# Kernel optimization log

Measured on AMD Instinct MI355X. Metric: run time of the kernel, lower is better.

The kernel has to match this reference:

```python
import jax, jax.numpy as jnp
import numpy as np

B, IN, H, OUT, N = 2048, 512, 512, 256, 32768

def setup_inputs() -> dict:
    key = jax.random.key(0)
    ks = jax.random.split(key, 12)
    s = 1.0 / np.sqrt(H)
    inp = {
        'x': jax.random.normal(ks[0], (B, IN), jnp.float32),
        'Wih0': jax.random.uniform(ks[1], (3 * H, IN), jnp.float32, -s, s),
        'Whh0': jax.random.uniform(ks[2], (3 * H, H), jnp.float32, -s, s),
        'bih0': jax.random.uniform(ks[3], (3 * H,), jnp.float32, -s, s),
        'bhh0': jax.random.uniform(ks[4], (3 * H,), jnp.float32, -s, s),
        'Wih1': jax.random.uniform(ks[5], (3 * H, H), jnp.float32, -s, s),
        'Whh1': jax.random.uniform(ks[6], (3 * H, H), jnp.float32, -s, s),
        'bih1': jax.random.uniform(ks[7], (3 * H,), jnp.float32, -s, s),
        'bhh1': jax.random.uniform(ks[8], (3 * H,), jnp.float32, -s, s),
        'Wout': jax.random.uniform(ks[9], (OUT, H), jnp.float32, -s, s),
        'bout': jax.random.uniform(ks[10], (OUT,), jnp.float32, -s, s),
        'pre_set_idx': jnp.sort(jax.random.randint(ks[11], (N,), 0, B)),
    }
    return inp


def _gru_layer(seq, Wih, Whh, bih, bhh):
    # seq: [B, T, D]; PyTorch GRU gate order: r, z, n
    h_dim = Whh.shape[1]
    xp = jnp.einsum('btd,gd->btg', seq, Wih) + bih  # [B, T, 3H]
    xr, xz, xn = jnp.split(xp, 3, axis=-1)
    Whr, Whz, Whn = jnp.split(Whh, 3, axis=0)
    bhr, bhz, bhn = jnp.split(bhh, 3)

    def step(h, xs):
        xr_t, xz_t, xn_t = xs
        r = jax.nn.sigmoid(xr_t + h @ Whr.T + bhr)
        z = jax.nn.sigmoid(xz_t + h @ Whz.T + bhz)
        n = jnp.tanh(xn_t + r * (h @ Whn.T + bhn))
        h_new = (1.0 - z) * n + z * h
        return h_new, h_new

    h0 = jnp.zeros((seq.shape[0], h_dim), seq.dtype)
    xs = (xr.transpose(1, 0, 2), xz.transpose(1, 0, 2), xn.transpose(1, 0, 2))
    _, ys = jax.lax.scan(step, h0, xs)  # ys: [T, B, H]
    return ys.transpose(1, 0, 2)


def reference(x, Wih0, Whh0, bih0, bhh0, Wih1, Whh1, bih1, bhh1, Wout, bout, pre_set_idx):
    psi_np = np.asarray(pre_set_idx)
    counts_np = np.bincount(psi_np, minlength=B)
    T = int(counts_np.max())  # scipy mode(...).count == max count (static w.r.t. seed)

    # replicate the single-step input T times (original cat loop)
    x_seq = jnp.broadcast_to(x[:, None, :], (B, T, x.shape[1]))
    y0 = _gru_layer(x_seq, Wih0, Whh0, bih0, bhh0)
    y1 = _gru_layer(y0, Wih1, Whh1, bih1, bhh1)  # [B, T, H]

    # masked gather: for batch i, keep first cnt[i] timesteps (pre_set_idx is sorted)
    counts = jnp.asarray(counts_np)
    starts = jnp.concatenate([jnp.zeros(1, counts.dtype), jnp.cumsum(counts)[:-1]])
    rank = jnp.arange(N) - starts[pre_set_idx]  # position within each group
    gather_idx = pre_set_idx * T + rank
    flat = y1.reshape(-1, H)  # [B*T, H]
    sel = flat[gather_idx]  # [N, H]
    return sel @ Wout.T + bout  # [N, OUT]
```

## Files before the change

### kernel.cpp

```cpp
#include <hip/hip_runtime.h>
#include <math.h>

#define Bn   2048
#define Hd   512
#define H3   1536
#define OUTD 256
#define Nn   32768
#define TMAX 48
#define Kd   512

typedef __attribute__((ext_vector_type(8))) short short8v;
typedef __attribute__((ext_vector_type(4))) float float4v;

__device__ __forceinline__ float sigm(float x) { return 1.0f / (1.0f + __expf(-x)); }

__device__ __forceinline__ short f2bf(float v) {
    union { float f; unsigned u; } a; a.f = v;
    unsigned r = a.u + 0x7fffu + ((a.u >> 16) & 1u);
    return (short)(r >> 16);
}
__device__ __forceinline__ float bf2f(short s) {
    union { float f; unsigned u; } a; a.u = ((unsigned)(unsigned short)s) << 16;
    return a.f;
}

__global__ void prologue(const int* __restrict__ psi, int* __restrict__ perm,
                         int* __restrict__ startsP, int* __restrict__ active) {
    __shared__ int hist[64];
    __shared__ int base[64];
    __shared__ int cur[64];
    __shared__ int cnt_s[Bn];
    __shared__ int start_s[Bn];
    const int tid = threadIdx.x;
    if (tid < 64) { hist[tid] = 0; cur[tid] = 0; }
    __syncthreads();
    for (int b = tid; b < Bn; b += 1024) {
        int lo = 0, hi = Nn;
        while (lo < hi) { int mid = (lo + hi) >> 1; if (psi[mid] < b) lo = mid + 1; else hi = mid; }
        int lb = lo;
        lo = 0; hi = Nn;
        while (lo < hi) { int mid = (lo + hi) >> 1; if (psi[mid] <= b) lo = mid + 1; else hi = mid; }
        int c = lo - lb;
        cnt_s[b] = c;
        start_s[b] = lb;
        atomicAdd(&hist[min(c, 63)], 1);
    }
    __syncthreads();
    if (tid == 0) {
        base[63] = 0;
        for (int c = 62; c >= 0; --c) base[c] = base[c + 1] + hist[c + 1];
    }
    __syncthreads();
    if (tid < 64) active[tid] = base[tid];
    for (int b = tid; b < Bn; b += 1024) {
        int c = min(cnt_s[b], 63);
        int pos = base[c] + atomicAdd(&cur[c], 1);
        perm[pos] = b;
        startsP[pos] = start_s[b];
    }
}

__global__ __launch_bounds__(256)
void split_kern(const float* __restrict__ src, short* __restrict__ hi,
                short* __restrict__ lo, int n) {
    int i = (blockIdx.x * 256 + threadIdx.x) * 4;
    if (i >= n) return;
    float4 v = *(const float4*)&src[i];
    float vv[4] = {v.x, v.y, v.z, v.w};
    short h4[4], l4[4];
    #pragma unroll
    for (int c = 0; c < 4; ++c) {
        short h = f2bf(vv[c]);
        h4[c] = h;
        l4[c] = f2bf(vv[c] - bf2f(h));
    }
    *(short4*)&hi[i] = make_short4(h4[0], h4[1], h4[2], h4[3]);
    *(short4*)&lo[i] = make_short4(l4[0], l4[1], l4[2], l4[3]);
}

__global__ __launch_bounds__(256)
void zeroh(short* __restrict__ a, short* __restrict__ b,
           short* __restrict__ c, short* __restrict__ d) {
    int i = (blockIdx.x * 256 + threadIdx.x) * 4;
    short4 z = make_short4(0, 0, 0, 0);
    *(short4*)&a[i] = z; *(short4*)&b[i] = z;
    *(short4*)&c[i] = z; *(short4*)&d[i] = z;
}

template<bool SPLIT_A>
__device__ __forceinline__ void gemm_tile(
    const short* __restrict__ Ahi, const short* __restrict__ Alo,
    const short* __restrict__ Whi, const short* __restrict__ Wlo,
    const float* __restrict__ bias, float* __restrict__ C,
    int m0, int n0, int ldC, short* lds) {
    short* ldsAhi = lds;
    short* ldsAlo = lds + 4096;
    short* ldsBhi = lds + 8192;
    short* ldsBlo = lds + 12288;
    const int tid = threadIdx.x;
    const int wid = tid >> 6, lane = tid & 63;
    const int wm = wid >> 1, wn = wid & 1;
    const int oi0 = tid * 2, oi1 = tid * 2 + 1;
    const int r0 = oi0 >> 2, c0 = oi0 & 3;
    const int r1 = oi1 >> 2, c1 = oi1 & 3;
    const int w0 = ((r0 >> 4) * 64 + (r0 & 15) + (c0 << 4)) * 8;
    const int w1 = ((r1 >> 4) * 64 + (r1 & 15) + (c1 << 4)) * 8;

    float4v acc[4][4] = {};
    int4 ah0, ah1, al0, al1, bh0, bh1, bl0, bl1;

#define LOADK(kt) do { const int k0 = (kt) * 32; \
    ah0 = *(const int4*)&Ahi[(size_t)(m0 + r0) * Kd + k0 + c0 * 8]; \
    ah1 = *(const int4*)&Ahi[(size_t)(m0 + r1) * Kd + k0 + c1 * 8]; \
    if constexpr (SPLIT_A) { \
        al0 = *(const int4*)&Alo[(size_t)(m0 + r0) * Kd + k0 + c0 * 8]; \
        al1 = *(const int4*)&Alo[(size_t)(m0 + r1) * Kd + k0 + c1 * 8]; } \
    bh0 = *(const int4*)&Whi[(size_t)(n0 + r0) * Kd + k0 + c0 * 8]; \
    bh1 = *(const int4*)&Whi[(size_t)(n0 + r1) * Kd + k0 + c1 * 8]; \
    bl0 = *(const int4*)&Wlo[(size_t)(n0 + r0) * Kd + k0 + c0 * 8]; \
    bl1 = *(const int4*)&Wlo[(size_t)(n0 + r1) * Kd + k0 + c1 * 8]; } while (0)

    LOADK(0);
    for (int kt = 0; kt < 16; ++kt) {
        __syncthreads();
        *(int4*)&ldsAhi[w0] = ah0; *(int4*)&ldsAhi[w1] = ah1;
        if constexpr (SPLIT_A) { *(int4*)&ldsAlo[w0] = al0; *(int4*)&ldsAlo[w1] = al1; }
        *(int4*)&ldsBhi[w0] = bh0; *(int4*)&ldsBhi[w1] = bh1;
        *(int4*)&ldsBlo[w0] = bl0; *(int4*)&ldsBlo[w1] = bl1;
        __syncthreads();
        if (kt < 15) LOADK(kt + 1);
        short8v afh[4], afl[4], bfh[4], bfl[4];
        #pragma unroll
        for (int mi = 0; mi < 4; ++mi) {
            afh[mi] = *(const short8v*)&ldsAhi[((wm * 4 + mi) * 64 + lane) * 8];
            if constexpr (SPLIT_A)
                afl[mi] = *(const short8v*)&ldsAlo[((wm * 4 + mi) * 64 + lane) * 8];
        }
        #pragma unroll
        for (int ni = 0; ni < 4; ++ni) {
            bfh[ni] = *(const short8v*)&ldsBhi[((wn * 4 + ni) * 64 + lane) * 8];
            bfl[ni] = *(const short8v*)&ldsBlo[((wn * 4 + ni) * 64 + lane) * 8];
        }
        #pragma unroll
        for (int mi = 0; mi < 4; ++mi)
            #pragma unroll
            for (int ni = 0; ni < 4; ++ni) {
                acc[mi][ni] = __builtin_amdgcn_mfma_f32_16x16x32_bf16(afh[mi], bfh[ni], acc[mi][ni], 0, 0, 0);
                acc[mi][ni] = __builtin_amdgcn_mfma_f32_16x16x32_bf16(afh[mi], bfl[ni], acc[mi][ni], 0, 0, 0);
                if constexpr (SPLIT_A)
                    acc[mi][ni] = __builtin_amdgcn_mfma_f32_16x16x32_bf16(afl[mi], bfh[ni], acc[mi][ni], 0, 0, 0);
            }
    }
#undef LOADK
    #pragma unroll
    for (int mi = 0; mi < 4; ++mi) {
        #pragma unroll
        for (int ni = 0; ni < 4; ++ni) {
            int row = m0 + wm * 64 + mi * 16 + ((lane >> 4) << 2);
            int col = n0 + wn * 64 + ni * 16 + (lane & 15);
            float bv = bias ? bias[col] : 0.0f;
            #pragma unroll
            for (int r = 0; r < 4; ++r)
                C[(size_t)(row + r) * ldC + col] = acc[mi][ni][r] + bv;
        }
    }
}

template<bool SPLIT_A>
__global__ __launch_bounds__(256)
void gemm_one(const short* __restrict__ Ahi, const short* __restrict__ Alo,
              const short* __restrict__ Whi, const short* __restrict__ Wlo,
              const float* __restrict__ bias, float* __restrict__ C, int ntn) {
    __shared__ short lds[16384];
    int m0 = (blockIdx.x / ntn) * 128, n0 = (blockIdx.x % ntn) * 128;
    gemm_tile<SPLIT_A>(Ahi, Alo, Whi, Wlo, bias, C, m0, n0, ntn * 128, lds);
}

__global__ __launch_bounds__(256)
void step_gemm(const short* __restrict__ h0hi, const short* __restrict__ h0lo,
               const short* __restrict__ h1hi, const short* __restrict__ h1lo,
               const short* __restrict__ Whh0hi, const short* __restrict__ Whh0lo,
               const short* __restrict__ Wih1hi, const short* __restrict__ Wih1lo,
               const short* __restrict__ Whh1hi, const short* __restrict__ Whh1lo,
               float* __restrict__ gg0, float* __restrict__ ggX1, float* __restrict__ ggH1,
               const int* __restrict__ active, int i) {
    __shared__ short lds[16384];
    const int part = blockIdx.x / 192;
    const int bid = blockIdx.x % 192;
    const int m0 = (bid / 12) * 128, n0 = (bid % 12) * 128;
    if (part == 0) {
        const int act = active[i];
        if (m0 >= act) return;
        gemm_tile<true>(h0hi, h0lo, Whh0hi, Whh0lo, nullptr, gg0, m0, n0, H3, lds);
    } else if (part == 1) {
        if (i < 1) return;
        const int act = active[i - 1];
        if (m0 >= act) return;
        gemm_tile<true>(h0hi, h0lo, Wih1hi, Wih1lo, nullptr, ggX1, m0, n0, H3, lds);
    } else {
        if (i < 1) return;
        const int act = active[i - 1];
        if (m0 >= act) return;
        gemm_tile<true>(h1hi, h1lo, Whh1hi, Whh1lo, nullptr, ggH1, m0, n0, H3, lds);
    }
}

__global__ __launch_bounds__(256)
void cell_step(const float* __restrict__ gg0, const float* __restrict__ ggX1,
               const float* __restrict__ ggH1, const float* __restrict__ xp0,
               const float* __restrict__ bhh0, const float* __restrict__ bih1,
               const float* __restrict__ bhh1,
               short* __restrict__ h0hi, short* __restrict__ h0lo,
               short* __restrict__ h1hi, short* __restrict__ h1lo,
               short* __restrict__ sel_h,
               const int* __restrict__ perm, const int* __restrict__ startsP,
               const int* __restrict__ active, int i) {
    const int part = blockIdx.x >> 10;
    const int idx = (((blockIdx.x & 1023) * 256) + threadIdx.x) * 4;
    const int m = idx >> 9;
    const int j = idx & 511;
    if (part == 0) {
        const int act = active[i];
        if (m >= act) return;
        const int bsrc = perm[m];
        float4 gr = *(const float4*)&gg0[(size_t)m * H3 + j];
        float4 gz = *(const float4*)&gg0[(size_t)m * H3 + 512 + j];
        float4 gn = *(const float4*)&gg0[(size_t)m * H3 + 1024 + j];
        float4 xr = *(const float4*)&xp0[(size_t)bsrc * H3 + j];
        float4 xz = *(const float4*)&xp0[(size_t)bsrc * H3 + 512 + j];
        float4 xn = *(const float4*)&xp0[(size_t)bsrc * H3 + 1024 + j];
        short4 hh = *(const short4*)&h0hi[(size_t)m * Hd + j];
        short4 hl = *(const short4*)&h0lo[(size_t)m * Hd + j];
        float grv[4] = {gr.x, gr.y, gr.z, gr.w}, gzv[4] = {gz.x, gz.y, gz.z, gz.w}, gnv[4] = {gn.x, gn.y, gn.z, gn.w};
        float xrv[4] = {xr.x, xr.y, xr.z, xr.w}, xzv[4] = {xz.x, xz.y, xz.z, xz.w}, xnv[4] = {xn.x, xn.y, xn.z, xn.w};
        short hhv[4] = {hh.x, hh.y, hh.z, hh.w}, hlv[4] = {hl.x, hl.y, hl.z, hl.w};
        short nh[4], nl[4];
        #pragma unroll
        for (int c = 0; c < 4; ++c) {
            float hp = bf2f(hhv[c]) + bf2f(hlv[c]);
            float r = sigm(xrv[c] + grv[c] + bhh0[j + c]);
            float z = sigm(xzv[c] + gzv[c] + bhh0[512 + j + c]);
            float n = tanhf(xnv[c] + r * (gnv[c] + bhh0[1024 + j + c]));
            float h = (1.0f - z) * n + z * hp;
            nh[c] = f2bf(h);
            nl[c] = f2bf(h - bf2f(nh[c]));
        }
        *(short4*)&h0hi[(size_t)m * Hd + j] = make_short4(nh[0], nh[1], nh[2], nh[3]);
        *(short4*)&h0lo[(size_t)m * Hd + j] = make_short4(nl[0], nl[1], nl[2], nl[3]);
    } else {
        if (i < 1) return;
        const int act = active[i - 1];
        if (m >= act) return;
        const int t = i - 1;
        float4 ar = *(const float4*)&ggX1[(size_t)m * H3 + j];
        float4 az = *(const float4*)&ggX1[(size_t)m * H3 + 512 + j];
        float4 an = *(const float4*)&ggX1[(size_t)m * H3 + 1024 + j];
        float4 br = *(const float4*)&ggH1[(size_t)m * H3 + j];
        float4 bz = *(const float4*)&ggH1[(size_t)m * H3 + 512 + j];
        float4 bn = *(const float4*)&ggH1[(size_t)m * H3 + 1024 + j];
        short4 hh = *(const short4*)&h1hi[(size_t)m * Hd + j];
        short4 hl = *(const short4*)&h1lo[(size_t)m * Hd + j];
        float arv[4] = {ar.x, ar.y, ar.z, ar.w}, azv[4] = {az.x, az.y, az.z, az.w}, anv[4] = {an.x, an.y, an.z, an.w};
        float brv[4] = {br.x, br.y, br.z, br.w}, bzv[4] = {bz.x, bz.y, bz.z, bz.w}, bnv[4] = {bn.x, bn.y, bn.z, bn.w};
        short hhv[4] = {hh.x, hh.y, hh.z, hh.w}, hlv[4] = {hl.x, hl.y, hl.z, hl.w};
        short nh[4], nl[4], sb[4];
        #pragma unroll
        for (int c = 0; c < 4; ++c) {
            float hp = bf2f(hhv[c]) + bf2f(hlv[c]);
            float r = sigm(arv[c] + bih1[j + c] + brv[c] + bhh1[j + c]);
            float z = sigm(azv[c] + bih1[512 + j + c] + bzv[c] + bhh1[512 + j + c]);
            float n = tanhf(anv[c] + bih1[1024 + j + c] + r * (bnv[c] + bhh1[1024 + j + c]));
            float h = (1.0f - z) * n + z * hp;
            nh[c] = f2bf(h);
            nl[c] = f2bf(h - bf2f(nh[c]));
            sb[c] = f2bf(h);
        }
        *(short4*)&h1hi[(size_t)m * Hd + j] = make_short4(nh[0], nh[1], nh[2], nh[3]);
        *(short4*)&h1lo[(size_t)m * Hd + j] = make_short4(nl[0], nl[1], nl[2], nl[3]);
        size_t orow = (size_t)startsP[m] + t;
        *(short4*)&sel_h[orow * Hd + j] = make_short4(sb[0], sb[1], sb[2], sb[3]);
    }
}

extern "C" void kernel_launch(void* const* d_in, const int* in_sizes, int n_in,
                              void* d_out, int out_size, void* d_ws, size_t ws_size,
                              hipStream_t stream) {
    (void)in_sizes; (void)n_in; (void)out_size; (void)ws_size;
    const float* x    = (const float*)d_in[0];
    const float* Wih0 = (const float*)d_in[1];
    const float* Whh0 = (const float*)d_in[2];
    const float* bih0 = (const float*)d_in[3];
    const float* bhh0 = (const float*)d_in[4];
    const float* Wih1 = (const float*)d_in[5];
    const float* Whh1 = (const float*)d_in[6];
    const float* bih1 = (const float*)d_in[7];
    const float* bhh1 = (const float*)d_in[8];
    const float* Wout = (const float*)d_in[9];
    const float* bout = (const float*)d_in[10];
    const int*   psi  = (const int*)d_in[11];
    float* out = (float*)d_out;

    char* p = (char*)d_ws;
    auto alloc = [&](size_t bytes) { char* r = p; p += (bytes + 255) & ~255ULL; return r; };
    short* xhi    = (short*)alloc((size_t)Bn * Kd * 2);
    short* xlo    = (short*)alloc((size_t)Bn * Kd * 2);
    short* Wih0hi = (short*)alloc((size_t)H3 * Kd * 2);
    short* Wih0lo = (short*)alloc((size_t)H3 * Kd * 2);
    short* Whh0hi = (short*)alloc((size_t)H3 * Kd * 2);
    short* Whh0lo = (short*)alloc((size_t)H3 * Kd * 2);
    short* Wih1hi = (short*)alloc((size_t)H3 * Kd * 2);
    short* Wih1lo = (short*)alloc((size_t)H3 * Kd * 2);
    short* Whh1hi = (short*)alloc((size_t)H3 * Kd * 2);
    short* Whh1lo = (short*)alloc((size_t)H3 * Kd * 2);
    short* Wouthi = (short*)alloc((size_t)OUTD * Kd * 2);
    short* Woutlo = (short*)alloc((size_t)OUTD * Kd * 2);
    float* xp0    = (float*)alloc((size_t)Bn * H3 * 4);
    float* gg0    = (float*)alloc((size_t)Bn * H3 * 4);
    float* ggX1   = (float*)alloc((size_t)Bn * H3 * 4);
    float* ggH1   = (float*)alloc((size_t)Bn * H3 * 4);
    short* h0hi   = (short*)alloc((size_t)Bn * Hd * 2);
    short* h0lo   = (short*)alloc((size_t)Bn * Hd * 2);
    short* h1hi   = (short*)alloc((size_t)Bn * Hd * 2);
    short* h1lo   = (short*)alloc((size_t)Bn * Hd * 2);
    short* sel_h  = (short*)alloc((size_t)Nn * Hd * 2);
    int* perm     = (int*)alloc(Bn * 4);
    int* startsP  = (int*)alloc(Bn * 4);
    int* active   = (int*)alloc(64 * 4);

    split_kern<<<1024, 256, 0, stream>>>(x, xhi, xlo, Bn * Kd);
    split_kern<<<768, 256, 0, stream>>>(Wih0, Wih0hi, Wih0lo, H3 * Kd);
    split_kern<<<768, 256, 0, stream>>>(Whh0, Whh0hi, Whh0lo, H3 * Kd);
    split_kern<<<768, 256, 0, stream>>>(Wih1, Wih1hi, Wih1lo, H3 * Kd);
    split_kern<<<768, 256, 0, stream>>>(Whh1, Whh1hi, Whh1lo, H3 * Kd);
    split_kern<<<128, 256, 0, stream>>>(Wout, Wouthi, Woutlo, OUTD * Kd);
    prologue<<<1, 1024, 0, stream>>>(psi, perm, startsP, active);
    zeroh<<<1024, 256, 0, stream>>>(h0hi, h0lo, h1hi, h1lo);

    gemm_one<true><<<192, 256, 0, stream>>>(xhi, xlo, Wih0hi, Wih0lo, bih0, xp0, 12);

    for (int i = 0; i <= TMAX; ++i) {
        step_gemm<<<576, 256, 0, stream>>>(h0hi, h0lo, h1hi, h1lo,
                                           Whh0hi, Whh0lo, Wih1hi, Wih1lo, Whh1hi, Whh1lo,
                                           gg0, ggX1, ggH1, active, i);
        cell_step<<<2048, 256, 0, stream>>>(gg0, ggX1, ggH1, xp0,
                                            bhh0, bih1, bhh1,
                                            h0hi, h0lo, h1hi, h1lo,
                                            sel_h, perm, startsP, active, i);
    }

    gemm_one<false><<<512, 256, 0, stream>>>(sel_h, nullptr, Wouthi, Woutlo, bout, out, 2);
}
```

Baseline: 1.553 ms.

## Fuse per-step GRU gate GEMMs with cell update using ping-pong hidden buffers

Replaces the separate step GEMM and elementwise cell kernels with one fused kernel per timestep. Each block computes the r, z and n gate tiles for a 32-column slice and applies the GRU update in registers, so the fp32 gate intermediates no longer round-trip through global memory. Layer-1 input and hidden weights for r/z are concatenated along K so one 1024-long reduction serves both. Hidden states are stored interleaved in double-buffered [B,1024] arrays, and x is pre-permuted so xp0 needs no per-step indirection. The cost is narrower N tiles per block, which means the A operand is reloaded more often and layer-1 blocks do twice as much K work as layer-0 blocks, giving uneven load.

```diff
diff --git a/kernel.cpp b/kernel.cpp
--- a/kernel.cpp
+++ b/kernel.cpp
@@ -23,6 +23,8 @@
     union { float f; unsigned u; } a; a.u = ((unsigned)(unsigned short)s) << 16;
     return a.f;
 }
+
+#define MF(acc, A, B) acc = __builtin_amdgcn_mfma_f32_16x16x32_bf16(A, B, acc, 0, 0, 0)
 
 __global__ void prologue(const int* __restrict__ psi, int* __restrict__ perm,
                          int* __restrict__ startsP, int* __restrict__ active) {
@@ -79,9 +81,49 @@
 }
 
 __global__ __launch_bounds__(256)
-void zeroh(short* __restrict__ a, short* __restrict__ b,
-           short* __restrict__ c, short* __restrict__ d) {
+void split_perm(const float* __restrict__ src, const int* __restrict__ perm,
+                short* __restrict__ hi, short* __restrict__ lo) {
     int i = (blockIdx.x * 256 + threadIdx.x) * 4;
+    int row = i >> 9, col = i & 511;
+    int srow = perm[row];
+    float4 v = *(const float4*)&src[(size_t)srow * 512 + col];
+    float vv[4] = {v.x, v.y, v.z, v.w};
+    short h4[4], l4[4];
+    #pragma unroll
+    for (int c = 0; c < 4; ++c) {
+        short h = f2bf(vv[c]);
+        h4[c] = h;
+        l4[c] = f2bf(vv[c] - bf2f(h));
+    }
+    *(short4*)&hi[i] = make_short4(h4[0], h4[1], h4[2], h4[3]);
+    *(short4*)&lo[i] = make_short4(l4[0], l4[1], l4[2], l4[3]);
+}
+
+__global__ __launch_bounds__(256)
+void pack_w1rz(const float* __restrict__ Wih1, const float* __restrict__ Whh1,
+               short* __restrict__ hi, short* __restrict__ lo) {
+    int i = (blockIdx.x * 256 + threadIdx.x) * 4;
+    int orow = i >> 10, k = i & 1023;
+    const float* s = (k < 512) ? &Wih1[(size_t)orow * 512 + k]
+                               : &Whh1[(size_t)orow * 512 + (k - 512)];
+    float4 v = *(const float4*)s;
+    float vv[4] = {v.x, v.y, v.z, v.w};
+    short h4[4], l4[4];
+    #pragma unroll
+    for (int c = 0; c < 4; ++c) {
+        short h = f2bf(vv[c]);
+        h4[c] = h;
+        l4[c] = f2bf(vv[c] - bf2f(h));
+    }
+    *(short4*)&hi[i] = make_short4(h4[0], h4[1], h4[2], h4[3]);
+    *(short4*)&lo[i] = make_short4(l4[0], l4[1], l4[2], l4[3]);
+}
+
+__global__ __launch_bounds__(256)
+void zero4(short* __restrict__ a, short* __restrict__ b,
+           short* __restrict__ c, short* __restrict__ d, int n) {
+    int i = (blockIdx.x * 256 + threadIdx.x) * 4;
+    if (i >= n) return;
     short4 z = make_short4(0, 0, 0, 0);
     *(short4*)&a[i] = z; *(short4*)&b[i] = z;
     *(short4*)&c[i] = z; *(short4*)&d[i] = z;
@@ -145,10 +187,9 @@
         for (int mi = 0; mi < 4; ++mi)
             #pragma unroll
             for (int ni = 0; ni < 4; ++ni) {
-                acc[mi][ni] = __builtin_amdgcn_mfma_f32_16x16x32_bf16(afh[mi], bfh[ni], acc[mi][ni], 0, 0, 0);
-                acc[mi][ni] = __builtin_amdgcn_mfma_f32_16x16x32_bf16(afh[mi], bfl[ni], acc[mi][ni], 0, 0, 0);
-                if constexpr (SPLIT_A)
-                    acc[mi][ni] = __builtin_amdgcn_mfma_f32_16x16x32_bf16(afl[mi], bfh[ni], acc[mi][ni], 0, 0, 0);
+                MF(acc[mi][ni], afh[mi], bfh[ni]);
+                MF(acc[mi][ni], afh[mi], bfl[ni]);
+                if constexpr (SPLIT_A) MF(acc[mi][ni], afl[mi], bfh[ni]);
             }
     }
 #undef LOADK
@@ -177,109 +218,194 @@
 }
 
 __global__ __launch_bounds__(256)
-void step_gemm(const short* __restrict__ h0hi, const short* __restrict__ h0lo,
-               const short* __restrict__ h1hi, const short* __restrict__ h1lo,
-               const short* __restrict__ Whh0hi, const short* __restrict__ Whh0lo,
-               const short* __restrict__ Wih1hi, const short* __restrict__ Wih1lo,
-               const short* __restrict__ Whh1hi, const short* __restrict__ Whh1lo,
-               float* __restrict__ gg0, float* __restrict__ ggX1, float* __restrict__ ggH1,
-               const int* __restrict__ active, int i) {
-    __shared__ short lds[16384];
-    const int part = blockIdx.x / 192;
-    const int bid = blockIdx.x % 192;
-    const int m0 = (bid / 12) * 128, n0 = (bid % 12) * 128;
+void fused_step(const short* __restrict__ OLDhi, const short* __restrict__ OLDlo,
+                short* __restrict__ NEWhi, short* __restrict__ NEWlo,
+                const short* __restrict__ W0hi, const short* __restrict__ W0lo,
+                const short* __restrict__ Wrzhi, const short* __restrict__ Wrzlo,
+                const short* __restrict__ Wnxhi, const short* __restrict__ Wnxlo,
+                const short* __restrict__ Wnhhi, const short* __restrict__ Wnhlo,
+                const float* __restrict__ xp0P, const float* __restrict__ bhh0,
+                const float* __restrict__ bih1, const float* __restrict__ bhh1,
+                short* __restrict__ sel_h, const int* __restrict__ startsP,
+                const int* __restrict__ active, int i) {
+    __shared__ short lds[14336];
+    const int tid = threadIdx.x;
+    const int bb = blockIdx.x;
+    const int part = (bb >= 256);
+    const int idx = bb & 255;
+    const int js = idx >> 4, mb = idx & 15;
+    const int m0 = mb * 128, j0 = js * 32;
+    const int wid = tid >> 6, lane = tid & 63;
+    const int wm = wid >> 1, wn = wid & 1;
+
+    short* ldsAhi = lds;
+    short* ldsAlo = lds + 4096;
+    short* ldsP   = lds + 8192;
+
+    const int oiA0 = tid * 2, oiA1 = tid * 2 + 1;
+    const int rA0 = oiA0 >> 2, cA0 = oiA0 & 3;
+    const int rA1 = oiA1 >> 2, cA1 = oiA1 & 3;
+    const int wA0 = ((rA0 >> 4) * 64 + (rA0 & 15) + (cA0 << 4)) * 8;
+    const int wA1 = ((rA1 >> 4) * 64 + (rA1 & 15) + (cA1 << 4)) * 8;
+
+    const short* aB0h = OLDhi + (size_t)(m0 + rA0) * 1024 + cA0 * 8;
+    const short* aB1h = OLDhi + (size_t)(m0 + rA1) * 1024 + cA1 * 8;
+    const short* aB0l = OLDlo + (size_t)(m0 + rA0) * 1024 + cA0 * 8;
+    const short* aB1l = OLDlo + (size_t)(m0 + rA1) * 1024 + cA1 * 8;
+
+    int wPq[3], pg[3], prw[3], poc[3];
+    #pragma unroll
+    for (int rep = 0; rep < 3; ++rep) {
+        int id2 = rep * 256 + tid;
+        int p = id2 >> 7, wi = id2 & 127;
+        int prow = wi >> 2, poct = wi & 3;
+        wPq[rep] = p * 1024 + ((prow >> 4) * 64 + (prow & 15) + (poct << 4)) * 8;
+        pg[rep] = p; prw[rep] = prow; poc[rep] = poct;
+    }
+
+    const int col = j0 + wn * 16 + (lane & 15);
+
+#define AFRAGS \
+    short8v afh[4], afl[4]; \
+    _Pragma("unroll") for (int mi = 0; mi < 4; ++mi) { \
+        afh[mi] = *(const short8v*)&ldsAhi[((wm * 4 + mi) * 64 + lane) * 8]; \
+        afl[mi] = *(const short8v*)&ldsAlo[((wm * 4 + mi) * 64 + lane) * 8]; }
+
+#define GATEB(ACC, G) { \
+    short8v bh = *(const short8v*)&ldsP[((G) * 2 + 0) * 1024 + (wn * 64 + lane) * 8]; \
+    short8v bl = *(const short8v*)&ldsP[((G) * 2 + 1) * 1024 + (wn * 64 + lane) * 8]; \
+    _Pragma("unroll") for (int mi = 0; mi < 4; ++mi) { \
+        MF(ACC[mi], afh[mi], bh); MF(ACC[mi], afh[mi], bl); MF(ACC[mi], afl[mi], bh); } }
+
     if (part == 0) {
         const int act = active[i];
         if (m0 >= act) return;
-        gemm_tile<true>(h0hi, h0lo, Whh0hi, Whh0lo, nullptr, gg0, m0, n0, H3, lds);
-    } else if (part == 1) {
-        if (i < 1) return;
-        const int act = active[i - 1];
-        if (m0 >= act) return;
-        gemm_tile<true>(h0hi, h0lo, Wih1hi, Wih1lo, nullptr, ggX1, m0, n0, H3, lds);
+        const short* pb[3];
+        #pragma unroll
+        for (int rep = 0; rep < 3; ++rep) {
+            const short* W = (pg[rep] & 1) ? W0lo : W0hi;
+            pb[rep] = W + (size_t)((pg[rep] >> 1) * 512 + j0 + prw[rep]) * 512 + poc[rep] * 8;
+        }
+        float4v aR[4] = {}, aZ[4] = {}, aN[4] = {};
+        int4 s0, s1, s2, s3, q0, q1, q2;
+        auto LOAD = [&](int kt) {
+            int k0 = kt * 32;
+            s0 = *(const int4*)(aB0h + k0); s1 = *(const int4*)(aB1h + k0);
+            s2 = *(const int4*)(aB0l + k0); s3 = *(const int4*)(aB1l + k0);
+            q0 = *(const int4*)(pb[0] + k0);
+            q1 = *(const int4*)(pb[1] + k0);
+            q2 = *(const int4*)(pb[2] + k0);
+        };
+        LOAD(0);
+        for (int kt = 0; kt < 16; ++kt) {
+            __syncthreads();
+            *(int4*)&ldsAhi[wA0] = s0; *(int4*)&ldsAhi[wA1] = s1;
+            *(int4*)&ldsAlo[wA0] = s2; *(int4*)&ldsAlo[wA1] = s3;
+            *(int4*)&ldsP[wPq[0]] = q0; *(int4*)&ldsP[wPq[1]] = q1; *(int4*)&ldsP[wPq[2]] = q2;
+            __syncthreads();
+            if (kt < 15) LOAD(kt + 1);
+            AFRAGS
+            GATEB(aR, 0)
+            GATEB(aZ, 1)
+            GATEB(aN, 2)
+        }
+        const float b_r = bhh0[col], b_z = bhh0[512 + col], b_n = bhh0[1024 + col];
+        #pragma unroll
+        for (int mi = 0; mi < 4; ++mi) {
+            int rowb = m0 + wm * 64 + mi * 16 + ((lane >> 4) << 2);
+            #pragma unroll
+            for (int r = 0; r < 4; ++r) {
+                int row = rowb + r;
+                float xr = xp0P[(size_t)row * H3 + col];
+                float xz = xp0P[(size_t)row * H3 + 512 + col];
+                float xn = xp0P[(size_t)row * H3 + 1024 + col];
+                float rr = sigm(xr + aR[mi][r] + b_r);
+                float zz = sigm(xz + aZ[mi][r] + b_z);
+                float nn = tanhf(xn + rr * (aN[mi][r] + b_n));
+                float hp = bf2f(OLDhi[(size_t)row * 1024 + col]) + bf2f(OLDlo[(size_t)row * 1024 + col]);
+                float h = (1.0f - zz) * nn + zz * hp;
+                short hh = f2bf(h);
+                NEWhi[(size_t)row * 1024 + col] = hh;
+                NEWlo[(size_t)row * 1024 + col] = f2bf(h - bf2f(hh));
+            }
+        }
     } else {
         if (i < 1) return;
         const int act = active[i - 1];
         if (m0 >= act) return;
-        gemm_tile<true>(h1hi, h1lo, Whh1hi, Whh1lo, nullptr, ggH1, m0, n0, H3, lds);
-    }
-}
-
-__global__ __launch_bounds__(256)
-void cell_step(const float* __restrict__ gg0, const float* __restrict__ ggX1,
-               const float* __restrict__ ggH1, const float* __restrict__ xp0,
-               const float* __restrict__ bhh0, const float* __restrict__ bih1,
-               const float* __restrict__ bhh1,
-               short* __restrict__ h0hi, short* __restrict__ h0lo,
-               short* __restrict__ h1hi, short* __restrict__ h1lo,
-               short* __restrict__ sel_h,
-               const int* __restrict__ perm, const int* __restrict__ startsP,
-               const int* __restrict__ active, int i) {
-    const int part = blockIdx.x >> 10;
-    const int idx = (((blockIdx.x & 1023) * 256) + threadIdx.x) * 4;
-    const int m = idx >> 9;
-    const int j = idx & 511;
-    if (part == 0) {
-        const int act = active[i];
-        if (m >= act) return;
-        const int bsrc = perm[m];
-        float4 gr = *(const float4*)&gg0[(size_t)m * H3 + j];
-        float4 gz = *(const float4*)&gg0[(size_t)m * H3 + 512 + j];
-        float4 gn = *(const float4*)&gg0[(size_t)m * H3 + 1024 + j];
-        float4 xr = *(const float4*)&xp0[(size_t)bsrc * H3 + j];
-        float4 xz = *(const float4*)&xp0[(size_t)bsrc * H3 + 512 + j];
-        float4 xn = *(const float4*)&xp0[(size_t)bsrc * H3 + 1024 + j];
-        short4 hh = *(const short4*)&h0hi[(size_t)m * Hd + j];
-        short4 hl = *(const short4*)&h0lo[(size_t)m * Hd + j];
-        float grv[4] = {gr.x, gr.y, gr.z, gr.w}, gzv[4] = {gz.x, gz.y, gz.z, gz.w}, gnv[4] = {gn.x, gn.y, gn.z, gn.w};
-        float xrv[4] = {xr.x, xr.y, xr.z, xr.w}, xzv[4] = {xz.x, xz.y, xz.z, xz.w}, xnv[4] = {xn.x, xn.y, xn.z, xn.w};
-        short hhv[4] = {hh.x, hh.y, hh.z, hh.w}, hlv[4] = {hl.x, hl.y, hl.z, hl.w};
-        short nh[4], nl[4];
-        #pragma unroll
-        for (int c = 0; c < 4; ++c) {
-            float hp = bf2f(hhv[c]) + bf2f(hlv[c]);
-            float r = sigm(xrv[c] + grv[c] + bhh0[j + c]);
-            float z = sigm(xzv[c] + gzv[c] + bhh0[512 + j + c]);
-            float n = tanhf(xnv[c] + r * (gnv[c] + bhh0[1024 + j + c]));
-            float h = (1.0f - z) * n + z * hp;
-            nh[c] = f2bf(h);
-            nl[c] = f2bf(h - bf2f(nh[c]));
-        }
-        *(short4*)&h0hi[(size_t)m * Hd + j] = make_short4(nh[0], nh[1], nh[2], nh[3]);
-        *(short4*)&h0lo[(size_t)m * Hd + j] = make_short4(nl[0], nl[1], nl[2], nl[3]);
-    } else {
-        if (i < 1) return;
-        const int act = active[i - 1];
-        if (m >= act) return;
         const int t = i - 1;
-        float4 ar = *(const float4*)&ggX1[(size_t)m * H3 + j];
-        float4 az = *(const float4*)&ggX1[(size_t)m * H3 + 512 + j];
-        float4 an = *(const float4*)&ggX1[(size_t)m * H3 + 1024 + j];
-        float4 br = *(const float4*)&ggH1[(size_t)m * H3 + j];
-        float4 bz = *(const float4*)&ggH1[(size_t)m * H3 + 512 + j];
-        float4 bn = *(const float4*)&ggH1[(size_t)m * H3 + 1024 + j];
-        short4 hh = *(const short4*)&h1hi[(size_t)m * Hd + j];
-        short4 hl = *(const short4*)&h1lo[(size_t)m * Hd + j];
-        float arv[4] = {ar.x, ar.y, ar.z, ar.w}, azv[4] = {az.x, az.y, az.z, az.w}, anv[4] = {an.x, an.y, an.z, an.w};
-        float brv[4] = {br.x, br.y, br.z, br.w}, bzv[4] = {bz.x, bz.y, bz.z, bz.w}, bnv[4] = {bn.x, bn.y, bn.z, bn.w};
-        short hhv[4] = {hh.x, hh.y, hh.z, hh.w}, hlv[4] = {hl.x, hl.y, hl.z, hl.w};
-        short nh[4], nl[4], sb[4];
-        #pragma unroll
-        for (int c = 0; c < 4; ++c) {
-            float hp = bf2f(hhv[c]) + bf2f(hlv[c]);
-            float r = sigm(arv[c] + bih1[j + c] + brv[c] + bhh1[j + c]);
-            float z = sigm(azv[c] + bih1[512 + j + c] + bzv[c] + bhh1[512 + j + c]);
-            float n = tanhf(anv[c] + bih1[1024 + j + c] + r * (bnv[c] + bhh1[1024 + j + c]));
-            float h = (1.0f - z) * n + z * hp;
-            nh[c] = f2bf(h);
-            nl[c] = f2bf(h - bf2f(nh[c]));
-            sb[c] = f2bf(h);
-        }
-        *(short4*)&h1hi[(size_t)m * Hd + j] = make_short4(nh[0], nh[1], nh[2], nh[3]);
-        *(short4*)&h1lo[(size_t)m * Hd + j] = make_short4(nl[0], nl[1], nl[2], nl[3]);
-        size_t orow = (size_t)startsP[m] + t;
-        *(short4*)&sel_h[orow * Hd + j] = make_short4(sb[0], sb[1], sb[2], sb[3]);
-    }
+        const short* pbRZ[3]; const short* pbNx[3]; const short* pbNh[3]; int isn[3];
+        #pragma unroll
+        for (int rep = 0; rep < 3; ++rep) {
+            int g = pg[rep] >> 1, hl = pg[rep] & 1;
+            isn[rep] = (g == 2);
+            const short* Wrz = hl ? Wrzlo : Wrzhi;
+            const short* Wx  = hl ? Wnxlo : Wnxhi;
+            const short* Wh  = hl ? Wnhlo : Wnhhi;
+            pbRZ[rep] = Wrz + (size_t)(min(g, 1) * 512 + j0 + prw[rep]) * 1024 + poc[rep] * 8;
+            pbNx[rep] = Wx + (size_t)(j0 + prw[rep]) * 512 + poc[rep] * 8;
+            pbNh[rep] = Wh + (size_t)(j0 + prw[rep]) * 512 + poc[rep] * 8;
+        }
+        float4v aR[4] = {}, aZ[4] = {}, aXn[4] = {}, aHn[4] = {};
+        int4 s0, s1, s2, s3, q0, q1, q2;
+        auto LOAD = [&](int kt) {
+            int k0 = kt * 32;
+            s0 = *(const int4*)(aB0h + k0); s1 = *(const int4*)(aB1h + k0);
+            s2 = *(const int4*)(aB0l + k0); s3 = *(const int4*)(aB1l + k0);
+            q0 = *(const int4*)(isn[0] ? ((kt < 16) ? pbNx[0] + k0 : pbNh[0] + (k0 - 512)) : pbRZ[0] + k0);
+            q1 = *(const int4*)(isn[1] ? ((kt < 16) ? pbNx[1] + k0 : pbNh[1] + (k0 - 512)) : pbRZ[1] + k0);
+            q2 = *(const int4*)(isn[2] ? ((kt < 16) ? pbNx[2] + k0 : pbNh[2] + (k0 - 512)) : pbRZ[2] + k0);
+        };
+        LOAD(0);
+        for (int kt = 0; kt < 16; ++kt) {
+            __syncthreads();
+            *(int4*)&ldsAhi[wA0] = s0; *(int4*)&ldsAhi[wA1] = s1;
+            *(int4*)&ldsAlo[wA0] = s2; *(int4*)&ldsAlo[wA1] = s3;
+            *(int4*)&ldsP[wPq[0]] = q0; *(int4*)&ldsP[wPq[1]] = q1; *(int4*)&ldsP[wPq[2]] = q2;
+            __syncthreads();
+            LOAD(kt + 1);
+            AFRAGS
+            GATEB(aR, 0)
+            GATEB(aZ, 1)
+            GATEB(aXn, 2)
+        }
+        for (int kt = 16; kt < 32; ++kt) {
+            __syncthreads();
+            *(int4*)&ldsAhi[wA0] = s0; *(int4*)&ldsAhi[wA1] = s1;
+            *(int4*)&ldsAlo[wA0] = s2; *(int4*)&ldsAlo[wA1] = s3;
+            *(int4*)&ldsP[wPq[0]] = q0; *(int4*)&ldsP[wPq[1]] = q1; *(int4*)&ldsP[wPq[2]] = q2;
+            __syncthreads();
+            if (kt < 31) LOAD(kt + 1);
+            AFRAGS
+            GATEB(aR, 0)
+            GATEB(aZ, 1)
+            GATEB(aHn, 2)
+        }
+        const float b_r = bih1[col] + bhh1[col];
+        const float b_z = bih1[512 + col] + bhh1[512 + col];
+        const float b_xn = bih1[1024 + col];
+        const float b_hn = bhh1[1024 + col];
+        #pragma unroll
+        for (int mi = 0; mi < 4; ++mi) {
+            int rowb = m0 + wm * 64 + mi * 16 + ((lane >> 4) << 2);
+            #pragma unroll
+            for (int r = 0; r < 4; ++r) {
+                int row = rowb + r;
+                float rr = sigm(aR[mi][r] + b_r);
+                float zz = sigm(aZ[mi][r] + b_z);
+                float nn = tanhf(aXn[mi][r] + b_xn + rr * (aHn[mi][r] + b_hn));
+                float hp = bf2f(OLDhi[(size_t)row * 1024 + 512 + col]) + bf2f(OLDlo[(size_t)row * 1024 + 512 + col]);
+                float h = (1.0f - zz) * nn + zz * hp;
+                short hh = f2bf(h);
+                NEWhi[(size_t)row * 1024 + 512 + col] = hh;
+                NEWlo[(size_t)row * 1024 + 512 + col] = f2bf(h - bf2f(hh));
+                if (row < act)
+                    sel_h[((size_t)startsP[row] + t) * Hd + col] = f2bf(h);
+            }
+        }
+    }
+#undef AFRAGS
+#undef GATEB
 }
 
 extern "C" void kernel_launch(void* const* d_in, const int* in_sizes, int n_in,
@@ -302,50 +428,52 @@
 
     char* p = (char*)d_ws;
     auto alloc = [&](size_t bytes) { char* r = p; p += (bytes + 255) & ~255ULL; return r; };
-    short* xhi    = (short*)alloc((size_t)Bn * Kd * 2);
-    short* xlo    = (short*)alloc((size_t)Bn * Kd * 2);
+    short* xPhi   = (short*)alloc((size_t)Bn * Kd * 2);
+    short* xPlo   = (short*)alloc((size_t)Bn * Kd * 2);
     short* Wih0hi = (short*)alloc((size_t)H3 * Kd * 2);
     short* Wih0lo = (short*)alloc((size_t)H3 * Kd * 2);
-    short* Whh0hi = (short*)alloc((size_t)H3 * Kd * 2);
-    short* Whh0lo = (short*)alloc((size_t)H3 * Kd * 2);
-    short* Wih1hi = (short*)alloc((size_t)H3 * Kd * 2);
-    short* Wih1lo = (short*)alloc((size_t)H3 * Kd * 2);
-    short* Whh1hi = (short*)alloc((size_t)H3 * Kd * 2);
-    short* Whh1lo = (short*)alloc((size_t)H3 * Kd * 2);
+    short* W0hi   = (short*)alloc((size_t)H3 * Kd * 2);
+    short* W0lo   = (short*)alloc((size_t)H3 * Kd * 2);
+    short* Wrzhi  = (short*)alloc((size_t)1024 * 1024 * 2);
+    short* Wrzlo  = (short*)alloc((size_t)1024 * 1024 * 2);
+    short* Wnxhi  = (short*)alloc((size_t)512 * 512 * 2);
+    short* Wnxlo  = (short*)alloc((size_t)512 * 512 * 2);
+    short* Wnhhi  = (short*)alloc((size_t)512 * 512 * 2);
+    short* Wnhlo  = (short*)alloc((size_t)512 * 512 * 2);
     short* Wouthi = (short*)alloc((size_t)OUTD * Kd * 2);
     short* Woutlo = (short*)alloc((size_t)OUTD * Kd * 2);
-    float* xp0    = (float*)alloc((size_t)Bn * H3 * 4);
-    float* gg0    = (float*)alloc((size_t)Bn * H3 * 4);
-    float* ggX1   = (float*)alloc((size_t)Bn * H3 * 4);
-    float* ggH1   = (float*)alloc((size_t)Bn * H3 * 4);
-    short* h0hi   = (short*)alloc((size_t)Bn * Hd * 2);
-    short* h0lo   = (short*)alloc((size_t)Bn * Hd * 2);
-    short* h1hi   = (short*)alloc((size_t)Bn * Hd * 2);
-    short* h1lo   = (short*)alloc((size_t)Bn * Hd * 2);
+    float* xp0P   = (float*)alloc((size_t)Bn * H3 * 4);
+    short* Aahi   = (short*)alloc((size_t)Bn * 1024 * 2);
+    short* Aalo   = (short*)alloc((size_t)Bn * 1024 * 2);
+    short* Abhi   = (short*)alloc((size_t)Bn * 1024 * 2);
+    short* Ablo   = (short*)alloc((size_t)Bn * 1024 * 2);
     short* sel_h  = (short*)alloc((size_t)Nn * Hd * 2);
     int* perm     = (int*)alloc(Bn * 4);
     int* startsP  = (int*)alloc(Bn * 4);
     int* active   = (int*)alloc(64 * 4);
 
-    split_kern<<<1024, 256, 0, stream>>>(x, xhi, xlo, Bn * Kd);
+    prologue<<<1, 1024, 0, stream>>>(psi, perm, startsP, active);
+    split_perm<<<1024, 256, 0, stream>>>(x, perm, xPhi, xPlo);
     split_kern<<<768, 256, 0, stream>>>(Wih0, Wih0hi, Wih0lo, H3 * Kd);
-    split_kern<<<768, 256, 0, stream>>>(Whh0, Whh0hi, Whh0lo, H3 * Kd);
-    split_kern<<<768, 256, 0, stream>>>(Wih1, Wih1hi, Wih1lo, H3 * Kd);
-    split_kern<<<768, 256, 0, stream>>>(Whh1, Whh1hi, Whh1lo, H3 * Kd);
+    split_kern<<<768, 256, 0, stream>>>(Whh0, W0hi, W0lo, H3 * Kd);
+    pack_w1rz<<<1024, 256, 0, stream>>>(Wih1, Whh1, Wrzhi, Wrzlo);
+    split_kern<<<256, 256, 0, stream>>>(Wih1 + (size_t)1024 * 512, Wnxhi, Wnxlo, 512 * 512);
+    split_kern<<<256, 256, 0, stream>>>(Whh1 + (size_t)1024 * 512, Wnhhi, Wnhlo, 512 * 512);
     split_kern<<<128, 256, 0, stream>>>(Wout, Wouthi, Woutlo, OUTD * Kd);
-    prologue<<<1, 1024, 0, stream>>>(psi, perm, startsP, active);
-    zeroh<<<1024, 256, 0, stream>>>(h0hi, h0lo, h1hi, h1lo);
-
-    gemm_one<true><<<192, 256, 0, stream>>>(xhi, xlo, Wih0hi, Wih0lo, bih0, xp0, 12);
+    zero4<<<2048, 256, 0, stream>>>(Aahi, Aalo, Abhi, Ablo, Bn * 1024);
+
+    gemm_one<true><<<192, 256, 0, stream>>>(xPhi, xPlo, Wih0hi, Wih0lo, bih0, xp0P, 12);
 
     for (int i = 0; i <= TMAX; ++i) {
-        step_gemm<<<576, 256, 0, stream>>>(h0hi, h0lo, h1hi, h1lo,
-                                           Whh0hi, Whh0lo, Wih1hi, Wih1lo, Whh1hi, Whh1lo,
-                                           gg0, ggX1, ggH1, active, i);
-        cell_step<<<2048, 256, 0, stream>>>(gg0, ggX1, ggH1, xp0,
-                                            bhh0, bih1, bhh1,
-                                            h0hi, h0lo, h1hi, h1lo,
-                                            sel_h, perm, startsP, active, i);
+        const short* OLDhi = (i & 1) ? Abhi : Aahi;
+        const short* OLDlo = (i & 1) ? Ablo : Aalo;
+        short* NEWhi = (i & 1) ? Aahi : Abhi;
+        short* NEWlo = (i & 1) ? Aalo : Ablo;
+        fused_step<<<512, 256, 0, stream>>>(OLDhi, OLDlo, NEWhi, NEWlo,
+                                            W0hi, W0lo, Wrzhi, Wrzlo,
+                                            Wnxhi, Wnxlo, Wnhhi, Wnhlo,
+                                            xp0P, bhh0, bih1, bhh1,
+                                            sel_h, startsP, active, i);
     }
 
     gemm_one<false><<<512, 256, 0, stream>>>(sel_h, nullptr, Wouthi, Woutlo, bout, out, 2);
```

New measurement: 1.766 ms. +13.7%, slower.

## Use 512-thread GEMM tiles and pre-permute x to drop gather in cell step

Applied to the files above, without the earlier changes.

The GEMM tile moves from 4 waves with 4x4 MFMA subtiles to 8 waves with 4x2 subtiles. Each thread now stages one 16-byte chunk per operand per k-step, and step_gemm and gemm_one launch with 512 threads. Separately, x is permuted by perm while it is split to bf16, so the layer-0 input projection comes out already in sorted row order and cell_step reads it directly instead of through perm. This trades per-wave register and accumulator pressure for more waves per block and removes an indirect load, but each wave now gets less B-fragment reuse.

```diff
diff --git a/kernel.cpp b/kernel.cpp
--- a/kernel.cpp
+++ b/kernel.cpp
@@ -23,6 +23,8 @@
     union { float f; unsigned u; } a; a.u = ((unsigned)(unsigned short)s) << 16;
     return a.f;
 }
+
+#define MF(acc, A, B) acc = __builtin_amdgcn_mfma_f32_16x16x32_bf16(A, B, acc, 0, 0, 0)
 
 __global__ void prologue(const int* __restrict__ psi, int* __restrict__ perm,
                          int* __restrict__ startsP, int* __restrict__ active) {
@@ -43,6 +45,7 @@
         int c = lo - lb;
         cnt_s[b] = c;
         start_s[b] = lb;
+        lmax:;
         atomicAdd(&hist[min(c, 63)], 1);
     }
     __syncthreads();
@@ -79,6 +82,25 @@
 }
 
 __global__ __launch_bounds__(256)
+void split_perm(const float* __restrict__ src, const int* __restrict__ perm,
+                short* __restrict__ hi, short* __restrict__ lo) {
+    int i = (blockIdx.x * 256 + threadIdx.x) * 4;
+    int row = i >> 9, col = i & 511;
+    int srow = perm[row];
+    float4 v = *(const float4*)&src[(size_t)srow * 512 + col];
+    float vv[4] = {v.x, v.y, v.z, v.w};
+    short h4[4], l4[4];
+    #pragma unroll
+    for (int c = 0; c < 4; ++c) {
+        short h = f2bf(vv[c]);
+        h4[c] = h;
+        l4[c] = f2bf(vv[c] - bf2f(h));
+    }
+    *(short4*)&hi[i] = make_short4(h4[0], h4[1], h4[2], h4[3]);
+    *(short4*)&lo[i] = make_short4(l4[0], l4[1], l4[2], l4[3]);
+}
+
+__global__ __launch_bounds__(256)
 void zeroh(short* __restrict__ a, short* __restrict__ b,
            short* __restrict__ c, short* __restrict__ d) {
     int i = (blockIdx.x * 256 + threadIdx.x) * 4;
@@ -99,37 +121,34 @@
     short* ldsBlo = lds + 12288;
     const int tid = threadIdx.x;
     const int wid = tid >> 6, lane = tid & 63;
-    const int wm = wid >> 1, wn = wid & 1;
-    const int oi0 = tid * 2, oi1 = tid * 2 + 1;
-    const int r0 = oi0 >> 2, c0 = oi0 & 3;
-    const int r1 = oi1 >> 2, c1 = oi1 & 3;
-    const int w0 = ((r0 >> 4) * 64 + (r0 & 15) + (c0 << 4)) * 8;
-    const int w1 = ((r1 >> 4) * 64 + (r1 & 15) + (c1 << 4)) * 8;
-
-    float4v acc[4][4] = {};
-    int4 ah0, ah1, al0, al1, bh0, bh1, bl0, bl1;
+    const int wm = wid >> 2, wn = wid & 3;
+    const int sr = tid >> 2, so = tid & 3;
+    const int wOff = ((sr >> 4) * 64 + (sr & 15) + (so << 4)) * 8;
+
+    const short* gAhi = Ahi + (size_t)(m0 + sr) * Kd + so * 8;
+    const short* gAlo = SPLIT_A ? (Alo + (size_t)(m0 + sr) * Kd + so * 8) : nullptr;
+    const short* gBhi = Whi + (size_t)(n0 + sr) * Kd + so * 8;
+    const short* gBlo = Wlo + (size_t)(n0 + sr) * Kd + so * 8;
+
+    float4v acc[4][2] = {};
+    int4 vah, val, vbh, vbl;
 
 #define LOADK(kt) do { const int k0 = (kt) * 32; \
-    ah0 = *(const int4*)&Ahi[(size_t)(m0 + r0) * Kd + k0 + c0 * 8]; \
-    ah1 = *(const int4*)&Ahi[(size_t)(m0 + r1) * Kd + k0 + c1 * 8]; \
-    if constexpr (SPLIT_A) { \
-        al0 = *(const int4*)&Alo[(size_t)(m0 + r0) * Kd + k0 + c0 * 8]; \
-        al1 = *(const int4*)&Alo[(size_t)(m0 + r1) * Kd + k0 + c1 * 8]; } \
-    bh0 = *(const int4*)&Whi[(size_t)(n0 + r0) * Kd + k0 + c0 * 8]; \
-    bh1 = *(const int4*)&Whi[(size_t)(n0 + r1) * Kd + k0 + c1 * 8]; \
-    bl0 = *(const int4*)&Wlo[(size_t)(n0 + r0) * Kd + k0 + c0 * 8]; \
-    bl1 = *(const int4*)&Wlo[(size_t)(n0 + r1) * Kd + k0 + c1 * 8]; } while (0)
+    vah = *(const int4*)(gAhi + k0); \
+    if constexpr (SPLIT_A) val = *(const int4*)(gAlo + k0); \
+    vbh = *(const int4*)(gBhi + k0); \
+    vbl = *(const int4*)(gBlo + k0); } while (0)
 
     LOADK(0);
     for (int kt = 0; kt < 16; ++kt) {
         __syncthreads();
-        *(int4*)&ldsAhi[w0] = ah0; *(int4*)&ldsAhi[w1] = ah1;
-        if constexpr (SPLIT_A) { *(int4*)&ldsAlo[w0] = al0; *(int4*)&ldsAlo[w1] = al1; }
-        *(int4*)&ldsBhi[w0] = bh0; *(int4*)&ldsBhi[w1] = bh1;
-        *(int4*)&ldsBlo[w0] = bl0; *(int4*)&ldsBlo[w1] = bl1;
+        *(int4*)&ldsAhi[wOff] = vah;
+        if constexpr (SPLIT_A) *(int4*)&ldsAlo[wOff] = val;
+        *(int4*)&ldsBhi[wOff] = vbh;
+        *(int4*)&ldsBlo[wOff] = vbl;
         __syncthreads();
         if (kt < 15) LOADK(kt + 1);
-        short8v afh[4], afl[4], bfh[4], bfl[4];
+        short8v afh[4], afl[4], bfh[2], bfl[2];
         #pragma unroll
         for (int mi = 0; mi < 4; ++mi) {
             afh[mi] = *(const short8v*)&ldsAhi[((wm * 4 + mi) * 64 + lane) * 8];
@@ -137,27 +156,26 @@
                 afl[mi] = *(const short8v*)&ldsAlo[((wm * 4 + mi) * 64 + lane) * 8];
         }
         #pragma unroll
-        for (int ni = 0; ni < 4; ++ni) {
-            bfh[ni] = *(const short8v*)&ldsBhi[((wn * 4 + ni) * 64 + lane) * 8];
-            bfl[ni] = *(const short8v*)&ldsBlo[((wn * 4 + ni) * 64 + lane) * 8];
+        for (int ni = 0; ni < 2; ++ni) {
+            bfh[ni] = *(const short8v*)&ldsBhi[((wn * 2 + ni) * 64 + lane) * 8];
+            bfl[ni] = *(const short8v*)&ldsBlo[((wn * 2 + ni) * 64 + lane) * 8];
         }
         #pragma unroll
         for (int mi = 0; mi < 4; ++mi)
             #pragma unroll
-            for (int ni = 0; ni < 4; ++ni) {
-                acc[mi][ni] = __builtin_amdgcn_mfma_f32_16x16x32_bf16(afh[mi], bfh[ni], acc[mi][ni], 0, 0, 0);
-                acc[mi][ni] = __builtin_amdgcn_mfma_f32_16x16x32_bf16(afh[mi], bfl[ni], acc[mi][ni], 0, 0, 0);
-                if constexpr (SPLIT_A)
-                    acc[mi][ni] = __builtin_amdgcn_mfma_f32_16x16x32_bf16(afl[mi], bfh[ni], acc[mi][ni], 0, 0, 0);
+            for (int ni = 0; ni < 2; ++ni) {
+                MF(acc[mi][ni], afh[mi], bfh[ni]);
+                MF(acc[mi][ni], afh[mi], bfl[ni]);
+                if constexpr (SPLIT_A) MF(acc[mi][ni], afl[mi], bfh[ni]);
             }
     }
 #undef LOADK
     #pragma unroll
     for (int mi = 0; mi < 4; ++mi) {
         #pragma unroll
-        for (int ni = 0; ni < 4; ++ni) {
+        for (int ni = 0; ni < 2; ++ni) {
             int row = m0 + wm * 64 + mi * 16 + ((lane >> 4) << 2);
-            int col = n0 + wn * 64 + ni * 16 + (lane & 15);
+            int col = n0 + wn * 32 + ni * 16 + (lane & 15);
             float bv = bias ? bias[col] : 0.0f;
             #pragma unroll
             for (int r = 0; r < 4; ++r)
@@ -167,7 +185,7 @@
 }
 
 template<bool SPLIT_A>
-__global__ __launch_bounds__(256)
+__global__ __launch_bounds__(512)
 void gemm_one(const short* __restrict__ Ahi, const short* __restrict__ Alo,
               const short* __restrict__ Whi, const short* __restrict__ Wlo,
               const float* __restrict__ bias, float* __restrict__ C, int ntn) {
@@ -176,7 +194,7 @@
     gemm_tile<SPLIT_A>(Ahi, Alo, Whi, Wlo, bias, C, m0, n0, ntn * 128, lds);
 }
 
-__global__ __launch_bounds__(256)
+__global__ __launch_bounds__(512)
 void step_gemm(const short* __restrict__ h0hi, const short* __restrict__ h0lo,
                const short* __restrict__ h1hi, const short* __restrict__ h1lo,
                const short* __restrict__ Whh0hi, const short* __restrict__ Whh0lo,
@@ -207,13 +225,13 @@
 
 __global__ __launch_bounds__(256)
 void cell_step(const float* __restrict__ gg0, const float* __restrict__ ggX1,
-               const float* __restrict__ ggH1, const float* __restrict__ xp0,
+               const float* __restrict__ ggH1, const float* __restrict__ xp0P,
                const float* __restrict__ bhh0, const float* __restrict__ bih1,
                const float* __restrict__ bhh1,
                short* __restrict__ h0hi, short* __restrict__ h0lo,
                short* __restrict__ h1hi, short* __restrict__ h1lo,
                short* __restrict__ sel_h,
-               const int* __restrict__ perm, const int* __restrict__ startsP,
+               const int* __restrict__ startsP,
                const int* __restrict__ active, int i) {
     const int part = blockIdx.x >> 10;
     const int idx = (((blockIdx.x & 1023) * 256) + threadIdx.x) * 4;
@@ -222,13 +240,12 @@
     if (part == 0) {
         const int act = active[i];
         if (m >= act) return;
-        const int bsrc = perm[m];
         float4 gr = *(const float4*)&gg0[(size_t)m * H3 + j];
         float4 gz = *(const float4*)&gg0[(size_t)m * H3 + 512 + j];
         float4 gn = *(const float4*)&gg0[(size_t)m * H3 + 1024 + j];
-        float4 xr = *(const float4*)&xp0[(size_t)bsrc * H3 + j];
-        float4 xz = *(const float4*)&xp0[(size_t)bsrc * H3 + 512 + j];
-        float4 xn = *(const float4*)&xp0[(size_t)bsrc * H3 + 1024 + j];
+        float4 xr = *(const float4*)&xp0P[(size_t)m * H3 + j];
+        float4 xz = *(const float4*)&xp0P[(size_t)m * H3 + 512 + j];
+        float4 xn = *(const float4*)&xp0P[(size_t)m * H3 + 1024 + j];
         short4 hh = *(const short4*)&h0hi[(size_t)m * Hd + j];
         short4 hl = *(const short4*)&h0lo[(size_t)m * Hd + j];
         float grv[4] = {gr.x, gr.y, gr.z, gr.w}, gzv[4] = {gz.x, gz.y, gz.z, gz.w}, gnv[4] = {gn.x, gn.y, gn.z, gn.w};
@@ -302,8 +319,8 @@
 
     char* p = (char*)d_ws;
     auto alloc = [&](size_t bytes) { char* r = p; p += (bytes + 255) & ~255ULL; return r; };
-    short* xhi    = (short*)alloc((size_t)Bn * Kd * 2);
-    short* xlo    = (short*)alloc((size_t)Bn * Kd * 2);
+    short* xPhi   = (short*)alloc((size_t)Bn * Kd * 2);
+    short* xPlo   = (short*)alloc((size_t)Bn * Kd * 2);
     short* Wih0hi = (short*)alloc((size_t)H3 * Kd * 2);
     short* Wih0lo = (short*)alloc((size_t)H3 * Kd * 2);
     short* Whh0hi = (short*)alloc((size_t)H3 * Kd * 2);
@@ -314,7 +331,7 @@
     short* Whh1lo = (short*)alloc((size_t)H3 * Kd * 2);
     short* Wouthi = (short*)alloc((size_t)OUTD * Kd * 2);
     short* Woutlo = (short*)alloc((size_t)OUTD * Kd * 2);
-    float* xp0    = (float*)alloc((size_t)Bn * H3 * 4);
+    float* xp0P   = (float*)alloc((size_t)Bn * H3 * 4);
     float* gg0    = (float*)alloc((size_t)Bn * H3 * 4);
     float* ggX1   = (float*)alloc((size_t)Bn * H3 * 4);
     float* ggH1   = (float*)alloc((size_t)Bn * H3 * 4);
@@ -327,26 +344,26 @@
     int* startsP  = (int*)alloc(Bn * 4);
     int* active   = (int*)alloc(64 * 4);
 
-    split_kern<<<1024, 256, 0, stream>>>(x, xhi, xlo, Bn * Kd);
+    prologue<<<1, 1024, 0, stream>>>(psi, perm, startsP, active);
+    split_perm<<<1024, 256, 0, stream>>>(x, perm, xPhi, xPlo);
     split_kern<<<768, 256, 0, stream>>>(Wih0, Wih0hi, Wih0lo, H3 * Kd);
     split_kern<<<768, 256, 0, stream>>>(Whh0, Whh0hi, Whh0lo, H3 * Kd);
     split_kern<<<768, 256, 0, stream>>>(Wih1, Wih1hi, Wih1lo, H3 * Kd);
     split_kern<<<768, 256, 0, stream>>>(Whh1, Whh1hi, Whh1lo, H3 * Kd);
     split_kern<<<128, 256, 0, stream>>>(Wout, Wouthi, Woutlo, OUTD * Kd);
-    prologue<<<1, 1024, 0, stream>>>(psi, perm, startsP, active);
     zeroh<<<1024, 256, 0, stream>>>(h0hi, h0lo, h1hi, h1lo);
 
-    gemm_one<true><<<192, 256, 0, stream>>>(xhi, xlo, Wih0hi, Wih0lo, bih0, xp0, 12);
+    gemm_one<true><<<192, 512, 0, stream>>>(xPhi, xPlo, Wih0hi, Wih0lo, bih0, xp0P, 12);
 
     for (int i = 0; i <= TMAX; ++i) {
-        step_gemm<<<576, 256, 0, stream>>>(h0hi, h0lo, h1hi, h1lo,
+        step_gemm<<<576, 512, 0, stream>>>(h0hi, h0lo, h1hi, h1lo,
                                            Whh0hi, Whh0lo, Wih1hi, Wih1lo, Whh1hi, Whh1lo,
                                            gg0, ggX1, ggH1, active, i);
-        cell_step<<<2048, 256, 0, stream>>>(gg0, ggX1, ggH1, xp0,
+        cell_step<<<2048, 256, 0, stream>>>(gg0, ggX1, ggH1, xp0P,
                                             bhh0, bih1, bhh1,
                                             h0hi, h0lo, h1hi, h1lo,
-                                            sel_h, perm, startsP, active, i);
-    }
-
-    gemm_one<false><<<512, 256, 0, stream>>>(sel_h, nullptr, Wouthi, Woutlo, bout, out, 2);
-}
+                                            sel_h, startsP, active, i);
+    }
+
+    gemm_one<false><<<512, 512, 0, stream>>>(sel_h, nullptr, Wouthi, Woutlo, bout, out, 2);
+}
```

Result: slower. 1.600 ms (+3.0%).
